# Kernel optimization log

Hardware: AMD Instinct MI355X
Metric: run time of the kernel (lower is better)

The kernel has to match this reference:

```python
import jax, jax.numpy as jnp
import numpy as np
from jax import lax

N_KERNELS = 10000
IN_CH = 3
BATCH = 64
T_LEN = 1024
KSIZES = [7, 9, 11]
DILS = [1, 2, 4, 8, 16]
MAXK = max(KSIZES)

# Deterministic stand-in for torch's random per-kernel (size, dilation) draw.
_rng = np.random.default_rng(0)
_ks = np.array(KSIZES)[_rng.integers(0, len(KSIZES), N_KERNELS)]
_dil = np.array(DILS)[_rng.integers(0, len(DILS), N_KERNELS)]
GROUPS = []  # (kernel_size, dilation, static index array)
for _k in KSIZES:
    for _d in DILS:
        _idx = np.nonzero((_ks == _k) & (_dil == _d))[0]
        if _idx.size:
            GROUPS.append((_k, _d, _idx))
_PERM = np.concatenate([g[2] for g in GROUPS])  # grouped order -> original kernel id
INV_PERM = np.argsort(_PERM)                    # restore original kernel order


def setup_inputs() -> dict:
    key = jax.random.key(0)
    kx, kw, kb = jax.random.split(key, 3)
    x = jax.random.normal(kx, (BATCH, IN_CH, T_LEN), dtype=jnp.float32)
    # Weights padded to MAXK taps; taps beyond each kernel's size are zeroed
    # (zero taps do not change the conv output within the valid window).
    w = jax.random.normal(kw, (N_KERNELS, IN_CH, MAXK), dtype=jnp.float32)
    tap_mask = (np.arange(MAXK)[None, :] < _ks[:, None]).astype(np.float32)
    weights = w * jnp.asarray(tap_mask)[:, None, :]
    biases = 0.1 * jax.random.normal(kb, (N_KERNELS,), dtype=jnp.float32)
    return {"x": x, "weights": weights, "biases": biases}


def _rocket(x, weights, biases):
    # Group kernels by (size, dilation) -> <=15 batched convs instead of 10000 tiny ones.
    maxs, ppvs = [], []
    for k, d, idx in GROUPS:
        w = weights[idx, :, :k]                 # (G, C, k), idx is a static np array
        pad = (k - 1) * d // 2                  # 'same' padding (k odd -> exact)
        out = lax.conv_general_dilated(
            x, w, window_strides=(1,), padding=[(pad, pad)],
            rhs_dilation=(d,), dimension_numbers=("NCH", "OIH", "NCH"))
        out = out + biases[idx][None, :, None]  # (B, G, T)
        maxs.append(out.max(-1))                             # max pooling feature
        ppvs.append((out > 0).astype(jnp.float32).mean(-1))  # PPV feature
    mx = jnp.concatenate(maxs, 1)[:, INV_PERM]  # (B, N) in original kernel order
    pv = jnp.concatenate(ppvs, 1)[:, INV_PERM]
    # Interleave [max_0, ppv_0, max_1, ppv_1, ...] like torch.stack(features, dim=1)
    return jnp.stack([mx, pv], -1).reshape(x.shape[0], 2 * N_KERNELS)


def reference(x, weights, biases):
    return _rocket(x, weights, biases)
```

## Files before the change

kernel.cpp:

```cpp
#include <hip/hip_runtime.h>
#include <stdint.h>

#define N_KERNELS 10000
#define NCHUNK 56
#define CH_ALLOC 1312
#define PP_STRIDE (3 * CH_ALLOC)

typedef unsigned __int128 u128;
typedef __attribute__((ext_vector_type(8)))  short short8;
typedef __attribute__((ext_vector_type(16))) float floatx16;
typedef __attribute__((ext_vector_type(4)))  unsigned int uint4v;

struct KDraws { uint8_t k[N_KERNELS]; uint8_t d[N_KERNELS]; };

constexpr KDraws make_kd() {
    KDraws kd{};
    const u128 MULT = (((u128)0x2360ED051FC65DA4ULL) << 64) | 0x4385DF649FCCF645ULL;

    uint32_t hc = 0x43b0d7e5u;
    uint32_t pool[4] = {};
    for (int i = 0; i < 4; i++) {
        uint32_t v = 0u;
        v ^= hc; hc *= 0x931e8875u;
        v *= hc; v ^= v >> 16;
        pool[i] = v;
    }
    for (int s = 0; s < 4; s++)
        for (int dd = 0; dd < 4; dd++)
            if (s != dd) {
                uint32_t hv = pool[s];
                hv ^= hc; hc *= 0x931e8875u;
                hv *= hc; hv ^= hv >> 16;
                uint32_t rr = 0xca01f9ddu * pool[dd] - 0x4973f715u * hv;
                rr ^= rr >> 16;
                pool[dd] = rr;
            }
    uint32_t st[8] = {};
    uint32_t hcb = 0x8b51f9ddu;
    for (int i = 0; i < 8; i++) {
        uint32_t dv = pool[i & 3];
        dv ^= hcb; hcb *= 0x58f38dedu;
        dv *= hcb; dv ^= dv >> 16;
        st[i] = dv;
    }
    uint64_t w0 = (uint64_t)st[0] | ((uint64_t)st[1] << 32);
    uint64_t w1 = (uint64_t)st[2] | ((uint64_t)st[3] << 32);
    uint64_t w2 = (uint64_t)st[4] | ((uint64_t)st[5] << 32);
    uint64_t w3 = (uint64_t)st[6] | ((uint64_t)st[7] << 32);
    u128 initstate = (((u128)w0) << 64) | w1;
    u128 initseq   = (((u128)w2) << 64) | w3;

    u128 inc   = (initseq << 1) | 1;
    u128 state = 0;
    state = state * MULT + inc;
    state += initstate;
    state = state * MULT + inc;

    u128 s = state;
    for (int t = 0; t < 10000; ++t) {
        s = s * MULT + inc;
        uint64_t hi = (uint64_t)(s >> 64), lo = (uint64_t)s;
        unsigned rot = (unsigned)(hi >> 58);
        uint64_t v = hi ^ lo;
        uint64_t o = (v >> rot) | (v << ((64u - rot) & 63u));
        uint32_t d0 = (uint32_t)o;
        uint32_t d1 = (uint32_t)(o >> 32);
        int i0 = 2 * t, i1 = 2 * t + 1;
        if (i0 < 10000) kd.k[i0] = (uint8_t)(((uint64_t)d0 * 3u) >> 32);
        else            kd.d[i0 - 10000] = (uint8_t)(((uint64_t)d0 * 5u) >> 32);
        if (i1 < 10000) kd.k[i1] = (uint8_t)(((uint64_t)d1 * 3u) >> 32);
        else            kd.d[i1 - 10000] = (uint8_t)(((uint64_t)d1 * 5u) >> 32);
    }
    return kd;
}

constexpr KDraws kdr = make_kd();

struct Tables {
    alignas(16) int sched[4 * NCHUNK];
    int list[N_KERNELS];
};

constexpr Tables make_tables(const KDraws& kd) {
    Tables T{};
    int cnt[15] = {}, off[15] = {}, cur[15] = {};
    for (int i = 0; i < 10000; ++i) cnt[(int)kd.k[i] * 5 + (int)kd.d[i]]++;
    int o = 0;
    for (int g = 0; g < 15; ++g) { off[g] = o; cur[g] = o; o += cnt[g]; }
    for (int i = 0; i < 10000; ++i) {
        int g = (int)kd.k[i] * 5 + (int)kd.d[i];
        T.list[cur[g]++] = i;
    }
    const int kv[3] = {7, 9, 11};
    int ci = 0;
    for (int g = 0; g < 15; ++g) {
        int sz = cnt[g];
        for (int s2 = 0; s2 < sz; s2 += 256) {
            T.sched[4 * ci + 0] = kv[g / 5];
            T.sched[4 * ci + 1] = g % 5;
            T.sched[4 * ci + 2] = off[g] + s2;
            T.sched[4 * ci + 3] = (sz - s2 < 256) ? (sz - s2) : 256;
            ci++;
        }
    }
    for (; ci < NCHUNK; ci++) {
        T.sched[4 * ci + 0] = 0; T.sched[4 * ci + 1] = 0;
        T.sched[4 * ci + 2] = 0; T.sched[4 * ci + 3] = 0;
    }
    return T;
}

__constant__ Tables g_T = make_tables(kdr);

constexpr int count_chunks() {
    int cnt[15] = {};
    for (int i = 0; i < 10000; ++i) cnt[(int)kdr.k[i] * 5 + (int)kdr.d[i]]++;
    int ci = 0;
    for (int g = 0; g < 15; ++g)
        for (int s2 = 0; s2 < cnt[g]; s2 += 256) ci++;
    return ci;
}
constexpr int NCHUNK_REAL = count_chunks();

__device__ __forceinline__ uint16_t f32_to_bf16(float v) {
    uint32_t u = __builtin_bit_cast(uint32_t, v);
    return (uint16_t)((u + 0x7FFFu + ((u >> 16) & 1u)) >> 16);
}

__device__ __forceinline__ void stat16(const floatx16& C, float& mx, int& cnt) {
    float g0 = fmaxf(fmaxf(C[0],  C[1]),  C[2]);
    float g1 = fmaxf(fmaxf(C[3],  C[4]),  C[5]);
    float g2 = fmaxf(fmaxf(C[6],  C[7]),  C[8]);
    float g3 = fmaxf(fmaxf(C[9],  C[10]), C[11]);
    float g4 = fmaxf(fmaxf(C[12], C[13]), C[14]);
    float h0 = fmaxf(fmaxf(g0, g1), g2);
    float h1 = fmaxf(fmaxf(g3, g4), C[15]);
    mx = fmaxf(mx, fmaxf(h0, h1));
    #pragma unroll
    for (int i = 0; i < 16; i += 2) {
        int s0 = __builtin_bit_cast(int, C[i])     >> 31;
        int s1 = __builtin_bit_cast(int, C[i + 1]) >> 31;
        cnt += s0 + s1;
    }
}

template <int K, int D>
__device__ __forceinline__ void body(const float* __restrict__ x,
                                     const float* __restrict__ wgt,
                                     const float* __restrict__ bias,
                                     int lstart, int valid,
                                     float* __restrict__ out,
                                     short* __restrict__ xs,
                                     int b) {
    constexpr int H  = (K - 1) / 2;
    constexpr int Q  = 1024 / D;
    constexpr int S  = Q + 16;
    constexpr int OB = 8 - H;

    const int tid   = threadIdx.x;
    const int lane  = tid & 63;
    const int wave  = tid >> 6;
    const int jbase = (lane >> 5) * 8;
    const int m31   = lane & 31;
    const bool hi   = (jbase == 8);

    for (int idx = tid; idx < 3 * (CH_ALLOC + 8); idx += 256) {
        int c = idx / (CH_ALLOC + 8);
        int P = idx - c * (CH_ALLOC + 8);
        float v = 0.f;
        int y = P - 8;
        if (y >= 0) {
            int r = y / S;
            int q = y - r * S;
            if (r < D && q < Q) v = x[((size_t)b * 3 + c) * 1024 + r + D * q];
        }
        short hv = (short)f32_to_bf16(v);
        #pragma unroll
        for (int ph = 0; ph < 4; ++ph) {
            int ee = P - 2 * ph;
            if (ee >= 0 && ee < CH_ALLOC)
                xs[ph * PP_STRIDE + c * CH_ALLOC + ee] = hv;
        }
    }

    int i0 = wave * 64 + m31;
    int i1 = i0 + 32;
    int n0 = g_T.list[lstart + (i0 < valid ? i0 : valid - 1)];
    int n1 = g_T.list[lstart + (i1 < valid ? i1 : valid - 1)];
    float bv0 = bias[n0], bv1 = bias[n1];
    short8 whi[2][3];
    #pragma unroll
    for (int t2 = 0; t2 < 2; ++t2) {
        int n = t2 ? n1 : n0;
        float bv = t2 ? bv1 : bv0;
        #pragma unroll
        for (int c = 0; c < 3; ++c) {
            #pragma unroll
            for (int u = 0; u < 8; ++u) {
                int j = jbase + u;
                float wv = (j < 11) ? wgt[n * 33 + c * 11 + j] : 0.f;
                if (c == 2 && u == 7 && hi) wv = bv;
                whi[t2][c][u] = (short)f32_to_bf16(wv);
            }
        }
    }

    const floatx16 Zv = (floatx16)0.0f;
    const short one_bf16 = (short)0x3F80;

    __syncthreads();

    float mx0 = -3.402823466e38f, mx1 = -3.402823466e38f;
    int cnt0 = 0, cnt1 = 0;

    auto oddload = [](const short* cp) -> short8 {
        uint4v dv = __builtin_bit_cast(uint4v, *reinterpret_cast<const short8*>(cp));
        uint32_t d4 = *reinterpret_cast<const uint32_t*>(cp + 8);
        uint4v t;
        t[0] = (dv[0] >> 16) | (dv[1] << 16);
        t[1] = (dv[1] >> 16) | (dv[2] << 16);
        t[2] = (dv[2] >> 16) | (dv[3] << 16);
        t[3] = (dv[3] >> 16) | (d4    << 16);
        return __builtin_bit_cast(short8, t);
    };

    #pragma unroll 1
    for (int ri = 0; ri < 4; ++ri) {
        int rb, qb;
        if constexpr (D == 1)      { rb = 0;                   qb = 256 * ri + 8 * m31; }
        else if constexpr (D == 2) { rb = ri >> 1;             qb = (ri & 1) * 256 + 8 * m31; }
        else if constexpr (D == 4) { rb = ri;                  qb = 8 * m31; }
        else if constexpr (D == 8) { rb = 2 * ri + (m31 >> 4); qb = 8 * (m31 & 15); }
        else                       { rb = 4 * ri + (m31 >> 3); qb = 8 * (m31 & 7); }
        const int Abase = OB + rb * S + qb + jbase;

        #pragma unroll
        for (int p = 0; p < 8; ++p) {
            const int o8  = (OB + p) & 7;
            const bool od = (o8 & 1) != 0;
            const int ph  = (od ? o8 - 1 : o8) >> 1;
            const int L   = Abase + (p - o8);
            const short* bp = xs + ph * PP_STRIDE + L;
            short8 A0, A1, A2;
            if (!od) {
                A0 = *reinterpret_cast<const short8*>(bp);
                A1 = *reinterpret_cast<const short8*>(bp + CH_ALLOC);
                A2 = *reinterpret_cast<const short8*>(bp + 2 * CH_ALLOC);
            } else {
                A0 = oddload(bp);
                A1 = oddload(bp + CH_ALLOC);
                A2 = oddload(bp + 2 * CH_ALLOC);
            }
            A2[7] = hi ? one_bf16 : A2[7];

            floatx16 C0, C1;
            C0 = __builtin_amdgcn_mfma_f32_32x32x16_bf16(A0, whi[0][0], Zv, 0, 0, 0);
            C1 = __builtin_amdgcn_mfma_f32_32x32x16_bf16(A0, whi[1][0], Zv, 0, 0, 0);
            C0 = __builtin_amdgcn_mfma_f32_32x32x16_bf16(A1, whi[0][1], C0, 0, 0, 0);
            C1 = __builtin_amdgcn_mfma_f32_32x32x16_bf16(A1, whi[1][1], C1, 0, 0, 0);
            C0 = __builtin_amdgcn_mfma_f32_32x32x16_bf16(A2, whi[0][2], C0, 0, 0, 0);
            C1 = __builtin_amdgcn_mfma_f32_32x32x16_bf16(A2, whi[1][2], C1, 0, 0, 0);
            stat16(C0, mx0, cnt0);
            stat16(C1, mx1, cnt1);
        }
    }

    mx0  = fmaxf(mx0, __shfl_xor(mx0, 32));
    mx1  = fmaxf(mx1, __shfl_xor(mx1, 32));
    cnt0 += __shfl_xor(cnt0, 32);
    cnt1 += __shfl_xor(cnt1, 32);

    if (lane < 32) {
        float2* ob = reinterpret_cast<float2*>(out + (size_t)b * (2 * N_KERNELS));
        ob[n0] = make_float2(mx0, (float)(1024 + cnt0) * (1.0f / 1024.0f));
        ob[n1] = make_float2(mx1, (float)(1024 + cnt1) * (1.0f / 1024.0f));
    }
}

__global__ __launch_bounds__(256, 4)
void rocket_main(const float* __restrict__ x, const float* __restrict__ wgt,
                 const float* __restrict__ bias, float* __restrict__ out) {
    __shared__ __align__(16) short xs[4 * PP_STRIDE];
    int kc     = g_T.sched[4 * blockIdx.x + 0];
    int ld2    = g_T.sched[4 * blockIdx.x + 1];
    int lstart = g_T.sched[4 * blockIdx.x + 2];
    int valid  = g_T.sched[4 * blockIdx.x + 3];
    if (valid == 0) return;
    int b = blockIdx.y;
    switch (kc * 8 + ld2) {
        case 7*8+0:  body<7, 1 >(x, wgt, bias, lstart, valid, out, xs, b); break;
        case 7*8+1:  body<7, 2 >(x, wgt, bias, lstart, valid, out, xs, b); break;
        case 7*8+2:  body<7, 4 >(x, wgt, bias, lstart, valid, out, xs, b); break;
        case 7*8+3:  body<7, 8 >(x, wgt, bias, lstart, valid, out, xs, b); break;
        case 7*8+4:  body<7, 16>(x, wgt, bias, lstart, valid, out, xs, b); break;
        case 9*8+0:  body<9, 1 >(x, wgt, bias, lstart, valid, out, xs, b); break;
        case 9*8+1:  body<9, 2 >(x, wgt, bias, lstart, valid, out, xs, b); break;
        case 9*8+2:  body<9, 4 >(x, wgt, bias, lstart, valid, out, xs, b); break;
        case 9*8+3:  body<9, 8 >(x, wgt, bias, lstart, valid, out, xs, b); break;
        case 9*8+4:  body<9, 16>(x, wgt, bias, lstart, valid, out, xs, b); break;
        case 11*8+0: body<11,1 >(x, wgt, bias, lstart, valid, out, xs, b); break;
        case 11*8+1: body<11,2 >(x, wgt, bias, lstart, valid, out, xs, b); break;
        case 11*8+2: body<11,4 >(x, wgt, bias, lstart, valid, out, xs, b); break;
        case 11*8+3: body<11,8 >(x, wgt, bias, lstart, valid, out, xs, b); break;
        default:     body<11,16>(x, wgt, bias, lstart, valid, out, xs, b); break;
    }
}

extern "C" void kernel_launch(void* const* d_in, const int* in_sizes, int n_in,
                              void* d_out, int out_size, void* d_ws, size_t ws_size,
                              hipStream_t stream) {
    const float* x   = (const float*)d_in[0];
    const float* w   = (const float*)d_in[1];
    const float* b   = (const float*)d_in[2];
    float* out = (float*)d_out;
    (void)d_ws; (void)ws_size;

    hipLaunchKernelGGL(rocket_main, dim3(NCHUNK_REAL, 64), dim3(256), 0, stream,
                       x, w, b, out);
}
```

Baseline: 131.9 us.

## Process two batch rows per block, reusing weight registers and halving phase copies

Each block now handles a pair of batch samples, so the per-kernel weight and bias fragments loaded into registers are reused across two samples, and the grid's y dimension is halved. Shared memory still holds four phase-shifted bf16 copies, but now as two per sample instead of four for one sample, with the missing shifts rebuilt from 8-byte reads. The staging loop is simplified to zero-fill followed by scatter with shift-based index math. The cost is half as many blocks for latency hiding and longer serial work per block.

```diff
diff --git a/kernel.cpp b/kernel.cpp
--- a/kernel.cpp
+++ b/kernel.cpp
@@ -10,6 +10,7 @@
 typedef __attribute__((ext_vector_type(8)))  short short8;
 typedef __attribute__((ext_vector_type(16))) float floatx16;
 typedef __attribute__((ext_vector_type(4)))  unsigned int uint4v;
+typedef __attribute__((ext_vector_type(2)))  unsigned int uint2v;
 
 struct KDraws { uint8_t k[N_KERNELS]; uint8_t d[N_KERNELS]; };
 
@@ -151,9 +152,11 @@
                                      int lstart, int valid,
                                      float* __restrict__ out,
                                      short* __restrict__ xs,
-                                     int b) {
+                                     int bpair) {
     constexpr int H  = (K - 1) / 2;
     constexpr int Q  = 1024 / D;
+    constexpr int LQ = (Q == 1024) ? 10 : (Q == 512) ? 9 : (Q == 256) ? 8
+                     : (Q == 128) ? 7 : 6;
     constexpr int S  = Q + 16;
     constexpr int OB = 8 - H;
 
@@ -164,23 +167,30 @@
     const int m31   = lane & 31;
     const bool hi   = (jbase == 8);
 
-    for (int idx = tid; idx < 3 * (CH_ALLOC + 8); idx += 256) {
-        int c = idx / (CH_ALLOC + 8);
-        int P = idx - c * (CH_ALLOC + 8);
-        float v = 0.f;
-        int y = P - 8;
-        if (y >= 0) {
-            int r = y / S;
-            int q = y - r * S;
-            if (r < D && q < Q) v = x[((size_t)b * 3 + c) * 1024 + r + D * q];
-        }
+    {
+        uint4v z = (uint4v)0u;
+        uint4v* xv = reinterpret_cast<uint4v*>(xs);
+        #pragma unroll
+        for (int i = 0; i < 8; ++i) {
+            int idx = tid + i * 256;
+            if (idx < (4 * PP_STRIDE) / 8) xv[idx] = z;
+        }
+    }
+    __syncthreads();
+
+    for (int n = tid; n < 6144; n += 256) {
+        int c3   = n >> 10;
+        int t    = n & 1023;
+        int bsel = (c3 >= 3) ? 1 : 0;
+        int c    = c3 - 3 * bsel;
+        int r    = t >> LQ;
+        int q    = t & (Q - 1);
+        float v  = x[((size_t)(bpair * 2 + bsel) * 3 + c) * 1024 + r + D * q];
         short hv = (short)f32_to_bf16(v);
-        #pragma unroll
-        for (int ph = 0; ph < 4; ++ph) {
-            int ee = P - 2 * ph;
-            if (ee >= 0 && ee < CH_ALLOC)
-                xs[ph * PP_STRIDE + c * CH_ALLOC + ee] = hv;
-        }
+        int P    = 8 + (r << LQ) + (r << 4) + q;
+        short* sb = xs + ((bsel * 2 + 0) * 3 + c) * CH_ALLOC;
+        sb[P] = hv;
+        (sb + PP_STRIDE)[P - 2] = hv;
     }
 
     int i0 = wave * 64 + m31;
@@ -210,10 +220,16 @@
 
     __syncthreads();
 
-    float mx0 = -3.402823466e38f, mx1 = -3.402823466e38f;
-    int cnt0 = 0, cnt1 = 0;
-
-    auto oddload = [](const short* cp) -> short8 {
+    auto rd_e0 = [](const short* cp) -> short8 {
+        return *reinterpret_cast<const short8*>(cp);
+    };
+    auto rd_e4 = [](const short* cp) -> short8 {
+        uint2v a  = *reinterpret_cast<const uint2v*>(cp + 4);
+        uint2v b2 = *reinterpret_cast<const uint2v*>(cp + 8);
+        uint4v t; t[0] = a[0]; t[1] = a[1]; t[2] = b2[0]; t[3] = b2[1];
+        return __builtin_bit_cast(short8, t);
+    };
+    auto rd_o1 = [](const short* cp) -> short8 {
         uint4v dv = __builtin_bit_cast(uint4v, *reinterpret_cast<const short8*>(cp));
         uint32_t d4 = *reinterpret_cast<const uint32_t*>(cp + 8);
         uint4v t;
@@ -223,57 +239,87 @@
         t[3] = (dv[3] >> 16) | (d4    << 16);
         return __builtin_bit_cast(short8, t);
     };
+    auto rd_o5 = [](const short* cp) -> short8 {
+        uint2v a  = *reinterpret_cast<const uint2v*>(cp + 4);
+        uint2v b2 = *reinterpret_cast<const uint2v*>(cp + 8);
+        uint32_t d6 = *reinterpret_cast<const uint32_t*>(cp + 12);
+        uint4v t;
+        t[0] = (a[0]  >> 16) | (a[1]  << 16);
+        t[1] = (a[1]  >> 16) | (b2[0] << 16);
+        t[2] = (b2[0] >> 16) | (b2[1] << 16);
+        t[3] = (b2[1] >> 16) | (d6    << 16);
+        return __builtin_bit_cast(short8, t);
+    };
 
     #pragma unroll 1
-    for (int ri = 0; ri < 4; ++ri) {
-        int rb, qb;
-        if constexpr (D == 1)      { rb = 0;                   qb = 256 * ri + 8 * m31; }
-        else if constexpr (D == 2) { rb = ri >> 1;             qb = (ri & 1) * 256 + 8 * m31; }
-        else if constexpr (D == 4) { rb = ri;                  qb = 8 * m31; }
-        else if constexpr (D == 8) { rb = 2 * ri + (m31 >> 4); qb = 8 * (m31 & 15); }
-        else                       { rb = 4 * ri + (m31 >> 3); qb = 8 * (m31 & 7); }
-        const int Abase = OB + rb * S + qb + jbase;
-
-        #pragma unroll
-        for (int p = 0; p < 8; ++p) {
-            const int o8  = (OB + p) & 7;
-            const bool od = (o8 & 1) != 0;
-            const int ph  = (od ? o8 - 1 : o8) >> 1;
-            const int L   = Abase + (p - o8);
-            const short* bp = xs + ph * PP_STRIDE + L;
-            short8 A0, A1, A2;
-            if (!od) {
-                A0 = *reinterpret_cast<const short8*>(bp);
-                A1 = *reinterpret_cast<const short8*>(bp + CH_ALLOC);
-                A2 = *reinterpret_cast<const short8*>(bp + 2 * CH_ALLOC);
-            } else {
-                A0 = oddload(bp);
-                A1 = oddload(bp + CH_ALLOC);
-                A2 = oddload(bp + 2 * CH_ALLOC);
+    for (int bsel = 0; bsel < 2; ++bsel) {
+        const short* xb = xs + bsel * (2 * PP_STRIDE);
+        float mx0 = -3.402823466e38f, mx1 = -3.402823466e38f;
+        int cnt0 = 0, cnt1 = 0;
+
+        #pragma unroll 1
+        for (int ri = 0; ri < 4; ++ri) {
+            int rb, qb;
+            if constexpr (D == 1)      { rb = 0;                   qb = 256 * ri + 8 * m31; }
+            else if constexpr (D == 2) { rb = ri >> 1;             qb = (ri & 1) * 256 + 8 * m31; }
+            else if constexpr (D == 4) { rb = ri;                  qb = 8 * m31; }
+            else if constexpr (D == 8) { rb = 2 * ri + (m31 >> 4); qb = 8 * (m31 & 15); }
+            else                       { rb = 4 * ri + (m31 >> 3); qb = 8 * (m31 & 7); }
+            const int Abase = OB + rb * S + qb + jbase;
+
+            #pragma unroll
+            for (int p = 0; p < 8; ++p) {
+                const int o8 = (OB + p) & 7;
+                const int ph = (o8 >> 1) & 1;
+                const int L  = Abase + (p - o8);
+                const short* base = xb + ph * PP_STRIDE + L;
+                short8 A0, A1, A2;
+                if ((o8 & 1) == 0) {
+                    if ((o8 & 4) == 0) {
+                        A0 = rd_e0(base);
+                        A1 = rd_e0(base + CH_ALLOC);
+                        A2 = rd_e0(base + 2 * CH_ALLOC);
+                    } else {
+                        A0 = rd_e4(base);
+                        A1 = rd_e4(base + CH_ALLOC);
+                        A2 = rd_e4(base + 2 * CH_ALLOC);
+                    }
+                } else {
+                    if ((o8 & 4) == 0) {
+                        A0 = rd_o1(base);
+                        A1 = rd_o1(base + CH_ALLOC);
+                        A2 = rd_o1(base + 2 * CH_ALLOC);
+                    } else {
+                        A0 = rd_o5(base);
+                        A1 = rd_o5(base + CH_ALLOC);
+                        A2 = rd_o5(base + 2 * CH_ALLOC);
+                    }
+                }
+                A2[7] = hi ? one_bf16 : A2[7];
+
+                floatx16 C0, C1;
+                C0 = __builtin_amdgcn_mfma_f32_32x32x16_bf16(A0, whi[0][0], Zv, 0, 0, 0);
+                C1 = __builtin_amdgcn_mfma_f32_32x32x16_bf16(A0, whi[1][0], Zv, 0, 0, 0);
+                C0 = __builtin_amdgcn_mfma_f32_32x32x16_bf16(A1, whi[0][1], C0, 0, 0, 0);
+                C1 = __builtin_amdgcn_mfma_f32_32x32x16_bf16(A1, whi[1][1], C1, 0, 0, 0);
+                C0 = __builtin_amdgcn_mfma_f32_32x32x16_bf16(A2, whi[0][2], C0, 0, 0, 0);
+                C1 = __builtin_amdgcn_mfma_f32_32x32x16_bf16(A2, whi[1][2], C1, 0, 0, 0);
+                stat16(C0, mx0, cnt0);
+                stat16(C1, mx1, cnt1);
             }
-            A2[7] = hi ? one_bf16 : A2[7];
-
-            floatx16 C0, C1;
-            C0 = __builtin_amdgcn_mfma_f32_32x32x16_bf16(A0, whi[0][0], Zv, 0, 0, 0);
-            C1 = __builtin_amdgcn_mfma_f32_32x32x16_bf16(A0, whi[1][0], Zv, 0, 0, 0);
-            C0 = __builtin_amdgcn_mfma_f32_32x32x16_bf16(A1, whi[0][1], C0, 0, 0, 0);
-            C1 = __builtin_amdgcn_mfma_f32_32x32x16_bf16(A1, whi[1][1], C1, 0, 0, 0);
-            C0 = __builtin_amdgcn_mfma_f32_32x32x16_bf16(A2, whi[0][2], C0, 0, 0, 0);
-            C1 = __builtin_amdgcn_mfma_f32_32x32x16_bf16(A2, whi[1][2], C1, 0, 0, 0);
-            stat16(C0, mx0, cnt0);
-            stat16(C1, mx1, cnt1);
-        }
-    }
-
-    mx0  = fmaxf(mx0, __shfl_xor(mx0, 32));
-    mx1  = fmaxf(mx1, __shfl_xor(mx1, 32));
-    cnt0 += __shfl_xor(cnt0, 32);
-    cnt1 += __shfl_xor(cnt1, 32);
-
-    if (lane < 32) {
-        float2* ob = reinterpret_cast<float2*>(out + (size_t)b * (2 * N_KERNELS));
-        ob[n0] = make_float2(mx0, (float)(1024 + cnt0) * (1.0f / 1024.0f));
-        ob[n1] = make_float2(mx1, (float)(1024 + cnt1) * (1.0f / 1024.0f));
+        }
+
+        mx0  = fmaxf(mx0, __shfl_xor(mx0, 32));
+        mx1  = fmaxf(mx1, __shfl_xor(mx1, 32));
+        cnt0 += __shfl_xor(cnt0, 32);
+        cnt1 += __shfl_xor(cnt1, 32);
+
+        if (lane < 32) {
+            int b = bpair * 2 + bsel;
+            float2* ob = reinterpret_cast<float2*>(out + (size_t)b * (2 * N_KERNELS));
+            ob[n0] = make_float2(mx0, (float)(1024 + cnt0) * (1.0f / 1024.0f));
+            ob[n1] = make_float2(mx1, (float)(1024 + cnt1) * (1.0f / 1024.0f));
+        }
     }
 }
 
@@ -286,23 +332,23 @@
     int lstart = g_T.sched[4 * blockIdx.x + 2];
     int valid  = g_T.sched[4 * blockIdx.x + 3];
     if (valid == 0) return;
-    int b = blockIdx.y;
+    int bpair = blockIdx.y;
     switch (kc * 8 + ld2) {
-        case 7*8+0:  body<7, 1 >(x, wgt, bias, lstart, valid, out, xs, b); break;
-        case 7*8+1:  body<7, 2 >(x, wgt, bias, lstart, valid, out, xs, b); break;
-        case 7*8+2:  body<7, 4 >(x, wgt, bias, lstart, valid, out, xs, b); break;
-        case 7*8+3:  body<7, 8 >(x, wgt, bias, lstart, valid, out, xs, b); break;
-        case 7*8+4:  body<7, 16>(x, wgt, bias, lstart, valid, out, xs, b); break;
-        case 9*8+0:  body<9, 1 >(x, wgt, bias, lstart, valid, out, xs, b); break;
-        case 9*8+1:  body<9, 2 >(x, wgt, bias, lstart, valid, out, xs, b); break;
-        case 9*8+2:  body<9, 4 >(x, wgt, bias, lstart, valid, out, xs, b); break;
-        case 9*8+3:  body<9, 8 >(x, wgt, bias, lstart, valid, out, xs, b); break;
-        case 9*8+4:  body<9, 16>(x, wgt, bias, lstart, valid, out, xs, b); break;
-        case 11*8+0: body<11,1 >(x, wgt, bias, lstart, valid, out, xs, b); break;
-        case 11*8+1: body<11,2 >(x, wgt, bias, lstart, valid, out, xs, b); break;
-        case 11*8+2: body<11,4 >(x, wgt, bias, lstart, valid, out, xs, b); break;
-        case 11*8+3: body<11,8 >(x, wgt, bias, lstart, valid, out, xs, b); break;
-        default:     body<11,16>(x, wgt, bias, lstart, valid, out, xs, b); break;
+        case 7*8+0:  body<7, 1 >(x, wgt, bias, lstart, valid, out, xs, bpair); break;
+        case 7*8+1:  body<7, 2 >(x, wgt, bias, lstart, valid, out, xs, bpair); break;
+        case 7*8+2:  body<7, 4 >(x, wgt, bias, lstart, valid, out, xs, bpair); break;
+        case 7*8+3:  body<7, 8 >(x, wgt, bias, lstart, valid, out, xs, bpair); break;
+        case 7*8+4:  body<7, 16>(x, wgt, bias, lstart, valid, out, xs, bpair); break;
+        case 9*8+0:  body<9, 1 >(x, wgt, bias, lstart, valid, out, xs, bpair); break;
+        case 9*8+1:  body<9, 2 >(x, wgt, bias, lstart, valid, out, xs, bpair); break;
+        case 9*8+2:  body<9, 4 >(x, wgt, bias, lstart, valid, out, xs, bpair); break;
+        case 9*8+3:  body<9, 8 >(x, wgt, bias, lstart, valid, out, xs, bpair); break;
+        case 9*8+4:  body<9, 16>(x, wgt, bias, lstart, valid, out, xs, bpair); break;
+        case 11*8+0: body<11,1 >(x, wgt, bias, lstart, valid, out, xs, bpair); break;
+        case 11*8+1: body<11,2 >(x, wgt, bias, lstart, valid, out, xs, bpair); break;
+        case 11*8+2: body<11,4 >(x, wgt, bias, lstart, valid, out, xs, bpair); break;
+        case 11*8+3: body<11,8 >(x, wgt, bias, lstart, valid, out, xs, bpair); break;
+        default:     body<11,16>(x, wgt, bias, lstart, valid, out, xs, bpair); break;
     }
 }
 
@@ -315,6 +361,6 @@
     float* out = (float*)d_out;
     (void)d_ws; (void)ws_size;
 
-    hipLaunchKernelGGL(rocket_main, dim3(NCHUNK_REAL, 64), dim3(256), 0, stream,
+    hipLaunchKernelGGL(rocket_main, dim3(NCHUNK_REAL, 32), dim3(256), 0, stream,
                        x, w, b, out);
 }
```

Result: slower. 134.6 us (+2.0%).
